# Kernel optimization log

Measured on AMD Instinct MI355X. Metric: run time of the kernel, lower is better.

The kernel has to match this reference:

```python
import jax, jax.numpy as jnp
import numpy as np

N, E, G = 40000, 640000, 64
IN, H, OUT = 128, 256, 128


def setup_inputs() -> dict:
    key = jax.random.key(0)
    ks = jax.random.split(key, 8)
    x = jax.random.normal(ks[0], (N, IN), dtype=jnp.float32)
    edge_index = jax.random.randint(ks[1], (2, E), 0, N, dtype=jnp.int64)
    batch = jnp.sort(jax.random.randint(ks[2], (N,), 0, G, dtype=jnp.int64))
    glorot = lambda k, sh: jax.random.normal(k, sh, jnp.float32) * (1.0 / np.sqrt(sh[0]))
    return {
        "x": x,
        "edge_index": edge_index,
        "batch": batch,
        "W_in": glorot(ks[3], (IN, H)), "b_in": jnp.zeros((H,), jnp.float32),
        "W_mid": glorot(ks[4], (H, H)), "b_mid": jnp.zeros((H,), jnp.float32),
        "W_out": glorot(ks[5], (H, OUT)), "b_out": jnp.zeros((OUT,), jnp.float32),
        "W_cls": glorot(ks[6], (OUT, 2)), "b_cls": jnp.zeros((2,), jnp.float32),
    }


def _gcn_conv(x, src, dst, deg_inv_sqrt, W, b):
    # PyG GCNConv: h = x @ W; propagate with symmetric norm (self-loops added); + bias
    h = x @ W
    norm = deg_inv_sqrt[src] * deg_inv_sqrt[dst]            # [E]
    agg = jax.ops.segment_sum(norm[:, None] * h[src], dst, num_segments=x.shape[0])
    agg = agg + (deg_inv_sqrt * deg_inv_sqrt)[:, None] * h  # self-loop contribution
    return agg + b


def reference(x, edge_index, batch, W_in, b_in, W_mid, b_mid, W_out, b_out, W_cls, b_cls):
    src, dst = edge_index[0], edge_index[1]
    n = x.shape[0]
    # degree with self-loops (in-degree on dst, matching PyG default flow)
    deg = jax.ops.segment_sum(jnp.ones((src.shape[0],), x.dtype), dst, num_segments=n) + 1.0
    dis = jax.lax.rsqrt(deg)

    h = jax.nn.relu(_gcn_conv(x, src, dst, dis, W_in, b_in))
    h = jax.nn.relu(_gcn_conv(h, src, dst, dis, W_mid, b_mid))   # num_layers - 2 = 1 middle layer
    node_embeddings = _gcn_conv(h, src, dst, dis, W_out, b_out)

    # global mean pool over graphs
    counts = jax.ops.segment_sum(jnp.ones((n,), x.dtype), batch, num_segments=G)
    graph_embedding = jax.ops.segment_sum(node_embeddings, batch, num_segments=G) / jnp.maximum(counts, 1.0)[:, None]

    logits = graph_embedding @ W_cls + b_cls
    return (node_embeddings, graph_embedding, logits)
```

## Files before the change

### kernel.cpp

```cpp
#include <hip/hip_runtime.h>
#include <hip/hip_bf16.h>

#define Nn   40000
#define Ee   640000
#define Gg   64
#define INF  128
#define Hh   256
#define OUTF 128

#define NBLK_N 157

typedef _Float16 half8 __attribute__((ext_vector_type(8)));
typedef float    f32x4 __attribute__((ext_vector_type(4)));

__global__ __launch_bounds__(256) void k_count(const int* __restrict__ dst, int* __restrict__ cnt) {
    int e = blockIdx.x * 256 + threadIdx.x;
    if (e < Ee) atomicAdd(&cnt[dst[e]], 1);
}

__global__ __launch_bounds__(256) void k_dis(const int* __restrict__ cnt, float* __restrict__ dis) {
    int i = blockIdx.x * 256 + threadIdx.x;
    if (i < Nn) dis[i] = rsqrtf((float)cnt[i] + 1.0f);
}

__global__ __launch_bounds__(256)
void k_scan1(const int* __restrict__ cnt, int* __restrict__ offs, int* __restrict__ partial) {
    __shared__ int sm[256];
    int i = blockIdx.x * 256 + threadIdx.x;
    int v = (i < Nn) ? cnt[i] : 0;
    sm[threadIdx.x] = v;
    __syncthreads();
#pragma unroll
    for (int d = 1; d < 256; d <<= 1) {
        int t = (threadIdx.x >= d) ? sm[threadIdx.x - d] : 0;
        __syncthreads();
        sm[threadIdx.x] += t;
        __syncthreads();
    }
    if (i < Nn) offs[i] = sm[threadIdx.x] - v;
    if (threadIdx.x == 255) partial[blockIdx.x] = sm[255];
}

__global__ __launch_bounds__(256)
void k_scan2(int* __restrict__ partial) {
    __shared__ int sm[256];
    int v = (threadIdx.x < NBLK_N) ? partial[threadIdx.x] : 0;
    sm[threadIdx.x] = v;
    __syncthreads();
#pragma unroll
    for (int d = 1; d < 256; d <<= 1) {
        int t = (threadIdx.x >= d) ? sm[threadIdx.x - d] : 0;
        __syncthreads();
        sm[threadIdx.x] += t;
        __syncthreads();
    }
    if (threadIdx.x < NBLK_N) partial[threadIdx.x] = sm[threadIdx.x] - v;
}

__global__ __launch_bounds__(256)
void k_scan3(int* __restrict__ offs, const int* __restrict__ partial) {
    int i = blockIdx.x * 256 + threadIdx.x;
    if (i < Nn) offs[i] += partial[blockIdx.x];
    if (i == 0) offs[Nn] = Ee;
}

__global__ __launch_bounds__(256)
void k_fill(const int* __restrict__ src, const int* __restrict__ dst,
            const int* __restrict__ offs, int* __restrict__ cursor,
            unsigned short* __restrict__ src_sorted) {
    int e = blockIdx.x * 256 + threadIdx.x;
    if (e >= Ee) return;
    int d = dst[e];
    int pos = offs[d] + atomicAdd(&cursor[d], 1);
    src_sorted[pos] = (unsigned short)src[e];
}

__global__ __launch_bounds__(256)
void k_cvt_x(const float* __restrict__ x, _Float16* __restrict__ xh) {
    int i = (blockIdx.x * 256 + threadIdx.x) * 4;
    if (i >= Nn * INF) return;
    float4 v = *(const float4*)&x[i];
    xh[i + 0] = (_Float16)v.x;
    xh[i + 1] = (_Float16)v.y;
    xh[i + 2] = (_Float16)v.z;
    xh[i + 3] = (_Float16)v.w;
}

__global__ __launch_bounds__(256)
void k_cvt_wt(const float* __restrict__ W, _Float16* __restrict__ Wt, int K, int N) {
    int idx = blockIdx.x * 256 + threadIdx.x;
    if (idx >= K * N) return;
    int n = idx / K;
    int k = idx - n * K;
    Wt[idx] = (_Float16)W[(size_t)k * N + n];
}

__global__ __launch_bounds__(256)
void k_gemm_mfma(const _Float16* __restrict__ A, const _Float16* __restrict__ Wt,
                 const float* __restrict__ dis, _Float16* __restrict__ C16,
                 int M, int N, int K) {
    __shared__ _Float16 Alds[128 * 40];
    __shared__ _Float16 Blds[128 * 40];
    const int tid = threadIdx.x;
    const int lane = tid & 63;
    const int waveId = tid >> 6;
    const int waveRow = waveId >> 1;
    const int waveCol = waveId & 1;
    const int quad = lane >> 4;
    const int m16 = lane & 15;
    const int rowBase = blockIdx.x * 128;
    const int colBase = blockIdx.y * 128;

    const int sRow  = tid >> 1;
    const int sKoff = (tid & 1) * 16;

    int gr = rowBase + sRow; if (gr >= M) gr = M - 1;
    const int gn = colBase + sRow;

    f32x4 acc[4][4];
#pragma unroll
    for (int i = 0; i < 4; ++i)
#pragma unroll
        for (int j = 0; j < 4; ++j)
            acc[i][j] = (f32x4){0.0f, 0.0f, 0.0f, 0.0f};

    for (int k0 = 0; k0 < K; k0 += 32) {
        const uint4* ap = (const uint4*)(A  + (size_t)gr * K + k0 + sKoff);
        const uint4* bp = (const uint4*)(Wt + (size_t)gn * K + k0 + sKoff);
        uint4 a0 = ap[0], a1 = ap[1];
        uint4 b0 = bp[0], b1 = bp[1];
        __syncthreads();
        *(uint4*)&Alds[sRow * 40 + sKoff]     = a0;
        *(uint4*)&Alds[sRow * 40 + sKoff + 8] = a1;
        *(uint4*)&Blds[sRow * 40 + sKoff]     = b0;
        *(uint4*)&Blds[sRow * 40 + sKoff + 8] = b1;
        __syncthreads();

        half8 a_frag[4], b_frag[4];
#pragma unroll
        for (int rt = 0; rt < 4; ++rt)
            a_frag[rt] = *(const half8*)&Alds[(waveRow * 64 + rt * 16 + m16) * 40 + quad * 8];
#pragma unroll
        for (int ct = 0; ct < 4; ++ct)
            b_frag[ct] = *(const half8*)&Blds[(waveCol * 64 + ct * 16 + m16) * 40 + quad * 8];
#pragma unroll
        for (int rt = 0; rt < 4; ++rt)
#pragma unroll
            for (int ct = 0; ct < 4; ++ct)
                acc[rt][ct] = __builtin_amdgcn_mfma_f32_16x16x32_f16(
                    a_frag[rt], b_frag[ct], acc[rt][ct], 0, 0, 0);
    }

#pragma unroll
    for (int rt = 0; rt < 4; ++rt) {
        const int rb = rowBase + waveRow * 64 + rt * 16 + quad * 4;
#pragma unroll
        for (int r = 0; r < 4; ++r) {
            const int row = rb + r;
            if (row < M) {
                const float s = dis[row];
#pragma unroll
                for (int ct = 0; ct < 4; ++ct) {
                    const int col = colBase + waveCol * 64 + ct * 16 + m16;
                    C16[(size_t)row * N + col] = (_Float16)(s * acc[rt][ct][r]);
                }
            }
        }
    }
}

template <int HH, bool RELU, bool H16OUT>
__global__ __launch_bounds__(256)
void k_gatherh(const int* __restrict__ offs, const unsigned short* __restrict__ srcs,
               const float* __restrict__ dis, const _Float16* __restrict__ hp,
               const float* __restrict__ bias, void* __restrict__ outv) {
    constexpr int V = HH / 64;
    typedef _Float16 halfv __attribute__((ext_vector_type(V)));
    int n = blockIdx.x * 4 + (threadIdx.x >> 6);
    if (n >= Nn) return;
    int lane = threadIdx.x & 63;
    int col = lane * V;
    int b = __builtin_amdgcn_readfirstlane(offs[n]);
    int e = __builtin_amdgcn_readfirstlane(offs[n + 1]);

    float acc[V];
    {
        halfv sv = *(const halfv*)(hp + (size_t)n * HH + col);
#pragma unroll
        for (int j = 0; j < V; ++j) acc[j] = (float)sv[j];
    }

    int i = b;
    for (; i + 4 <= e; i += 4) {
        int s0 = srcs[i], s1 = srcs[i + 1], s2 = srcs[i + 2], s3 = srcs[i + 3];
        halfv v0 = *(const halfv*)(hp + (size_t)s0 * HH + col);
        halfv v1 = *(const halfv*)(hp + (size_t)s1 * HH + col);
        halfv v2 = *(const halfv*)(hp + (size_t)s2 * HH + col);
        halfv v3 = *(const halfv*)(hp + (size_t)s3 * HH + col);
#pragma unroll
        for (int j = 0; j < V; ++j)
            acc[j] += (float)v0[j] + (float)v1[j] + (float)v2[j] + (float)v3[j];
    }
    for (; i < e; ++i) {
        int s0 = srcs[i];
        halfv v0 = *(const halfv*)(hp + (size_t)s0 * HH + col);
#pragma unroll
        for (int j = 0; j < V; ++j) acc[j] += (float)v0[j];
    }

    float dn = dis[n];
    float r[V];
#pragma unroll
    for (int j = 0; j < V; ++j) {
        r[j] = dn * acc[j] + bias[col + j];
        if (RELU) r[j] = fmaxf(r[j], 0.0f);
    }
    if constexpr (H16OUT) {
        halfv hv;
#pragma unroll
        for (int j = 0; j < V; ++j) hv[j] = (_Float16)r[j];
        *(halfv*)((_Float16*)outv + (size_t)n * HH + col) = hv;
    } else {
        if constexpr (V == 4) {
            *(float4*)((float*)outv + (size_t)n * HH + col) = make_float4(r[0], r[1], r[2], r[3]);
        } else {
            *(float2*)((float*)outv + (size_t)n * HH + col) = make_float2(r[0], r[1]);
        }
    }
}

__global__ __launch_bounds__(256)
void k_pool_accum(const float* __restrict__ emb, const int* __restrict__ batch,
                  float* __restrict__ ge_accum) {
    int n0 = blockIdx.x * 64;
    int nend = min(n0 + 64, Nn);
    int sub = threadIdx.x >> 6;
    int col = (threadIdx.x & 63) * 2;
    float ax = 0.0f, ay = 0.0f;
    int cur_g = -1;
    for (int n = n0 + sub; n < nend; n += 4) {
        int g = batch[n];
        if (g != cur_g) {
            if (cur_g >= 0) {
                unsafeAtomicAdd(&ge_accum[cur_g * OUTF + col], ax);
                unsafeAtomicAdd(&ge_accum[cur_g * OUTF + col + 1], ay);
            }
            cur_g = g; ax = 0.0f; ay = 0.0f;
        }
        float2 v = *(const float2*)&emb[(size_t)n * OUTF + col];
        ax += v.x; ay += v.y;
    }
    if (cur_g >= 0) {
        unsafeAtomicAdd(&ge_accum[cur_g * OUTF + col], ax);
        unsafeAtomicAdd(&ge_accum[cur_g * OUTF + col + 1], ay);
    }
}

__global__ __launch_bounds__(256)
void k_pool_div(const float* __restrict__ ge_accum, const int* __restrict__ batch,
                float* __restrict__ ge) {
    int idx = blockIdx.x * 256 + threadIdx.x;
    if (idx >= Gg * OUTF) return;
    int g = idx >> 7;
    int lo = 0, hi = Nn;
    while (lo < hi) { int mid = (lo + hi) >> 1; if (batch[mid] < g) lo = mid + 1; else hi = mid; }
    int start = lo;
    hi = Nn;
    while (lo < hi) { int mid = (lo + hi) >> 1; if (batch[mid] < g + 1) lo = mid + 1; else hi = mid; }
    float cnt = (float)(lo - start);
    ge[idx] = ge_accum[idx] / fmaxf(cnt, 1.0f);
}

__global__ __launch_bounds__(128)
void k_logits(const float* __restrict__ ge, const float* __restrict__ Wc,
              const float* __restrict__ bc, float* __restrict__ out) {
    int t = threadIdx.x;
    int g = t >> 1, c = t & 1;
    float s = bc[c];
    for (int k = 0; k < 128; ++k) s += ge[g * 128 + k] * Wc[k * 2 + c];
    out[t] = s;
}

extern "C" void kernel_launch(void* const* d_in, const int* in_sizes, int n_in,
                              void* d_out, int out_size, void* d_ws, size_t ws_size,
                              hipStream_t stream) {
    const float* x     = (const float*)d_in[0];
    const int*   ei    = (const int*)d_in[1];
    const int*   batch = (const int*)d_in[2];
    const float* W_in  = (const float*)d_in[3];
    const float* b_in  = (const float*)d_in[4];
    const float* W_mid = (const float*)d_in[5];
    const float* b_mid = (const float*)d_in[6];
    const float* W_out = (const float*)d_in[7];
    const float* b_out = (const float*)d_in[8];
    const float* W_cls = (const float*)d_in[9];
    const float* b_cls = (const float*)d_in[10];

    const int* src = ei;
    const int* dst = ei + Ee;

    float* ws = (float*)d_ws;
    float* dis      = ws;
    int*   cnt      = (int*)(ws + 40000);
    int*   offs     = (int*)(ws + 80000);
    int*   partial  = (int*)(ws + 120064);
    float* ge_accum = ws + 120256;
    unsigned short* src_sorted = (unsigned short*)(ws + 128448);
    _Float16* xh     = (_Float16*)(ws + 448448);
    _Float16* Wt_in  = (_Float16*)(ws + 3008448);
    _Float16* Wt_mid = (_Float16*)(ws + 3024832);
    _Float16* Wt_out = (_Float16*)(ws + 3057600);
    _Float16* hA     = (_Float16*)(ws + 3073984);
    _Float16* actA   = (_Float16*)(ws + 8193984);

    float* out    = (float*)d_out;
    float* ge_out = out + (size_t)Nn * OUTF;
    float* lg_out = ge_out + Gg * OUTF;

    const int nBlkE = (Ee + 255) / 256;
    const int gRows = (Nn + 127) / 128;
    const int nBlkG = (Nn + 3) / 4;

    hipMemsetAsync(cnt, 0, Nn * sizeof(int), stream);
    k_count<<<nBlkE, 256, 0, stream>>>(dst, cnt);
    k_dis<<<NBLK_N, 256, 0, stream>>>(cnt, dis);
    k_scan1<<<NBLK_N, 256, 0, stream>>>(cnt, offs, partial);
    k_scan2<<<1, 256, 0, stream>>>(partial);
    k_scan3<<<NBLK_N, 256, 0, stream>>>(offs, partial);
    hipMemsetAsync(cnt, 0, Nn * sizeof(int), stream);
    k_fill<<<nBlkE, 256, 0, stream>>>(src, dst, offs, cnt, src_sorted);

    k_cvt_x<<<(Nn * INF / 4 + 255) / 256, 256, 0, stream>>>(x, xh);
    k_cvt_wt<<<(INF * Hh + 255) / 256, 256, 0, stream>>>(W_in, Wt_in, INF, Hh);
    k_cvt_wt<<<(Hh * Hh + 255) / 256, 256, 0, stream>>>(W_mid, Wt_mid, Hh, Hh);
    k_cvt_wt<<<(Hh * OUTF + 255) / 256, 256, 0, stream>>>(W_out, Wt_out, Hh, OUTF);

    k_gemm_mfma<<<dim3(gRows, Hh / 128), 256, 0, stream>>>(xh, Wt_in, dis, hA, Nn, Hh, INF);
    k_gatherh<Hh, true, true><<<nBlkG, 256, 0, stream>>>(offs, src_sorted, dis, hA, b_in, actA);

    k_gemm_mfma<<<dim3(gRows, Hh / 128), 256, 0, stream>>>(actA, Wt_mid, dis, hA, Nn, Hh, Hh);
    k_gatherh<Hh, true, true><<<nBlkG, 256, 0, stream>>>(offs, src_sorted, dis, hA, b_mid, actA);

    k_gemm_mfma<<<dim3(gRows, OUTF / 128), 256, 0, stream>>>(actA, Wt_out, dis, hA, Nn, OUTF, Hh);
    k_gatherh<OUTF, false, false><<<nBlkG, 256, 0, stream>>>(offs, src_sorted, dis, hA, b_out, out);

    hipMemsetAsync(ge_accum, 0, Gg * OUTF * sizeof(float), stream);
    k_pool_accum<<<(Nn + 63) / 64, 256, 0, stream>>>(out, batch, ge_accum);
    k_pool_div<<<(Gg * OUTF + 255) / 256, 256, 0, stream>>>(ge_accum, batch, ge_out);
    k_logits<<<1, 128, 0, stream>>>(ge_out, W_cls, b_cls, lg_out);
}
```

Baseline: 361.8 us.

## Merge small setup and pooling kernels, drop memsets, use nontemporal gather loads

Folds the degree-inverse computation and the counter reset into the first scan kernel. It also merges the x and weight conversions plus the zeroing of the pool accumulator into one launch, and merges the pool division with the logits into a single-block kernel. This removes several kernel launches and two memsets. Separately, the neighbor gathers now use nontemporal loads, which risks losing cache reuse of the feature rows that are read repeatedly.

```diff
diff --git a/kernel.cpp b/kernel.cpp
--- a/kernel.cpp
+++ b/kernel.cpp
@@ -18,16 +18,17 @@
     if (e < Ee) atomicAdd(&cnt[dst[e]], 1);
 }
 
-__global__ __launch_bounds__(256) void k_dis(const int* __restrict__ cnt, float* __restrict__ dis) {
-    int i = blockIdx.x * 256 + threadIdx.x;
-    if (i < Nn) dis[i] = rsqrtf((float)cnt[i] + 1.0f);
-}
-
-__global__ __launch_bounds__(256)
-void k_scan1(const int* __restrict__ cnt, int* __restrict__ offs, int* __restrict__ partial) {
+__global__ __launch_bounds__(256)
+void k_scan1(int* __restrict__ cnt, int* __restrict__ offs, int* __restrict__ partial,
+             float* __restrict__ dis) {
     __shared__ int sm[256];
     int i = blockIdx.x * 256 + threadIdx.x;
-    int v = (i < Nn) ? cnt[i] : 0;
+    int v = 0;
+    if (i < Nn) {
+        v = cnt[i];
+        dis[i] = rsqrtf((float)v + 1.0f);
+        cnt[i] = 0;
+    }
     sm[threadIdx.x] = v;
     __syncthreads();
 #pragma unroll
@@ -76,23 +77,36 @@
 }
 
 __global__ __launch_bounds__(256)
-void k_cvt_x(const float* __restrict__ x, _Float16* __restrict__ xh) {
-    int i = (blockIdx.x * 256 + threadIdx.x) * 4;
-    if (i >= Nn * INF) return;
-    float4 v = *(const float4*)&x[i];
-    xh[i + 0] = (_Float16)v.x;
-    xh[i + 1] = (_Float16)v.y;
-    xh[i + 2] = (_Float16)v.z;
-    xh[i + 3] = (_Float16)v.w;
-}
-
-__global__ __launch_bounds__(256)
-void k_cvt_wt(const float* __restrict__ W, _Float16* __restrict__ Wt, int K, int N) {
-    int idx = blockIdx.x * 256 + threadIdx.x;
-    if (idx >= K * N) return;
-    int n = idx / K;
-    int k = idx - n * K;
-    Wt[idx] = (_Float16)W[(size_t)k * N + n];
+void k_cvt_all(const float* __restrict__ x, _Float16* __restrict__ xh,
+               const float* __restrict__ W_in,  _Float16* __restrict__ Wt_in,
+               const float* __restrict__ W_mid, _Float16* __restrict__ Wt_mid,
+               const float* __restrict__ W_out, _Float16* __restrict__ Wt_out,
+               float* __restrict__ ge_accum) {
+    int bid = blockIdx.x;
+    int tid = threadIdx.x;
+    if (bid < 5000) {
+        int i = (bid * 256 + tid) * 4;
+        float4 v = *(const float4*)&x[i];
+        xh[i + 0] = (_Float16)v.x;
+        xh[i + 1] = (_Float16)v.y;
+        xh[i + 2] = (_Float16)v.z;
+        xh[i + 3] = (_Float16)v.w;
+    } else if (bid < 5128) {
+        int idx = (bid - 5000) * 256 + tid;
+        int n = idx >> 7, k = idx & 127;
+        Wt_in[idx] = (_Float16)W_in[(size_t)k * Hh + n];
+    } else if (bid < 5384) {
+        int idx = (bid - 5128) * 256 + tid;
+        int n = idx >> 8, k = idx & 255;
+        Wt_mid[idx] = (_Float16)W_mid[(size_t)k * Hh + n];
+    } else if (bid < 5512) {
+        int idx = (bid - 5384) * 256 + tid;
+        int n = idx >> 8, k = idx & 255;
+        Wt_out[idx] = (_Float16)W_out[(size_t)k * OUTF + n];
+    } else {
+        int idx = (bid - 5512) * 256 + tid;
+        ge_accum[idx] = 0.0f;
+    }
 }
 
 __global__ __launch_bounds__(256)
@@ -183,6 +197,17 @@
     int b = __builtin_amdgcn_readfirstlane(offs[n]);
     int e = __builtin_amdgcn_readfirstlane(offs[n + 1]);
 
+    auto ldrow = [&](int s) -> halfv {
+        const _Float16* p = hp + (size_t)s * HH + col;
+        if constexpr (V == 4) {
+            unsigned long long u = __builtin_nontemporal_load((const unsigned long long*)p);
+            return __builtin_bit_cast(halfv, u);
+        } else {
+            unsigned int u = __builtin_nontemporal_load((const unsigned int*)p);
+            return __builtin_bit_cast(halfv, u);
+        }
+    };
+
     float acc[V];
     {
         halfv sv = *(const halfv*)(hp + (size_t)n * HH + col);
@@ -193,17 +218,16 @@
     int i = b;
     for (; i + 4 <= e; i += 4) {
         int s0 = srcs[i], s1 = srcs[i + 1], s2 = srcs[i + 2], s3 = srcs[i + 3];
-        halfv v0 = *(const halfv*)(hp + (size_t)s0 * HH + col);
-        halfv v1 = *(const halfv*)(hp + (size_t)s1 * HH + col);
-        halfv v2 = *(const halfv*)(hp + (size_t)s2 * HH + col);
-        halfv v3 = *(const halfv*)(hp + (size_t)s3 * HH + col);
+        halfv v0 = ldrow(s0);
+        halfv v1 = ldrow(s1);
+        halfv v2 = ldrow(s2);
+        halfv v3 = ldrow(s3);
 #pragma unroll
         for (int j = 0; j < V; ++j)
             acc[j] += (float)v0[j] + (float)v1[j] + (float)v2[j] + (float)v3[j];
     }
     for (; i < e; ++i) {
-        int s0 = srcs[i];
-        halfv v0 = *(const halfv*)(hp + (size_t)s0 * HH + col);
+        halfv v0 = ldrow(srcs[i]);
 #pragma unroll
         for (int j = 0; j < V; ++j) acc[j] += (float)v0[j];
     }
@@ -257,28 +281,32 @@
 }
 
 __global__ __launch_bounds__(256)
-void k_pool_div(const float* __restrict__ ge_accum, const int* __restrict__ batch,
-                float* __restrict__ ge) {
-    int idx = blockIdx.x * 256 + threadIdx.x;
-    if (idx >= Gg * OUTF) return;
-    int g = idx >> 7;
-    int lo = 0, hi = Nn;
-    while (lo < hi) { int mid = (lo + hi) >> 1; if (batch[mid] < g) lo = mid + 1; else hi = mid; }
-    int start = lo;
-    hi = Nn;
-    while (lo < hi) { int mid = (lo + hi) >> 1; if (batch[mid] < g + 1) lo = mid + 1; else hi = mid; }
-    float cnt = (float)(lo - start);
-    ge[idx] = ge_accum[idx] / fmaxf(cnt, 1.0f);
-}
-
-__global__ __launch_bounds__(128)
-void k_logits(const float* __restrict__ ge, const float* __restrict__ Wc,
-              const float* __restrict__ bc, float* __restrict__ out) {
+void k_pool_fin(const float* __restrict__ ge_accum, const int* __restrict__ batch,
+                const float* __restrict__ Wc, const float* __restrict__ bc,
+                float* __restrict__ ge_out, float* __restrict__ lg_out) {
+    __shared__ float ge_s[Gg * OUTF];
+    __shared__ int seg[Gg + 1];
     int t = threadIdx.x;
-    int g = t >> 1, c = t & 1;
-    float s = bc[c];
-    for (int k = 0; k < 128; ++k) s += ge[g * 128 + k] * Wc[k * 2 + c];
-    out[t] = s;
+    if (t <= Gg) {
+        int lo = 0, hi = Nn;
+        while (lo < hi) { int mid = (lo + hi) >> 1; if (batch[mid] < t) lo = mid + 1; else hi = mid; }
+        seg[t] = lo;
+    }
+    __syncthreads();
+    for (int idx = t; idx < Gg * OUTF; idx += 256) {
+        int g = idx >> 7;
+        float cnt = (float)(seg[g + 1] - seg[g]);
+        float v = ge_accum[idx] / fmaxf(cnt, 1.0f);
+        ge_s[idx] = v;
+        ge_out[idx] = v;
+    }
+    __syncthreads();
+    if (t < 128) {
+        int g = t >> 1, c = t & 1;
+        float s = bc[c];
+        for (int k = 0; k < 128; ++k) s += ge_s[g * 128 + k] * Wc[k * 2 + c];
+        lg_out[t] = s;
+    }
 }
 
 extern "C" void kernel_launch(void* const* d_in, const int* in_sizes, int n_in,
@@ -321,19 +349,14 @@
     const int gRows = (Nn + 127) / 128;
     const int nBlkG = (Nn + 3) / 4;
 
-    hipMemsetAsync(cnt, 0, Nn * sizeof(int), stream);
+    (void)hipMemsetAsync(cnt, 0, Nn * sizeof(int), stream);
     k_count<<<nBlkE, 256, 0, stream>>>(dst, cnt);
-    k_dis<<<NBLK_N, 256, 0, stream>>>(cnt, dis);
-    k_scan1<<<NBLK_N, 256, 0, stream>>>(cnt, offs, partial);
+    k_scan1<<<NBLK_N, 256, 0, stream>>>(cnt, offs, partial, dis);
     k_scan2<<<1, 256, 0, stream>>>(partial);
     k_scan3<<<NBLK_N, 256, 0, stream>>>(offs, partial);
-    hipMemsetAsync(cnt, 0, Nn * sizeof(int), stream);
     k_fill<<<nBlkE, 256, 0, stream>>>(src, dst, offs, cnt, src_sorted);
 
-    k_cvt_x<<<(Nn * INF / 4 + 255) / 256, 256, 0, stream>>>(x, xh);
-    k_cvt_wt<<<(INF * Hh + 255) / 256, 256, 0, stream>>>(W_in, Wt_in, INF, Hh);
-    k_cvt_wt<<<(Hh * Hh + 255) / 256, 256, 0, stream>>>(W_mid, Wt_mid, Hh, Hh);
-    k_cvt_wt<<<(Hh * OUTF + 255) / 256, 256, 0, stream>>>(W_out, Wt_out, Hh, OUTF);
+    k_cvt_all<<<5544, 256, 0, stream>>>(x, xh, W_in, Wt_in, W_mid, Wt_mid, W_out, Wt_out, ge_accum);
 
     k_gemm_mfma<<<dim3(gRows, Hh / 128), 256, 0, stream>>>(xh, Wt_in, dis, hA, Nn, Hh, INF);
     k_gatherh<Hh, true, true><<<nBlkG, 256, 0, stream>>>(offs, src_sorted, dis, hA, b_in, actA);
@@ -344,8 +367,6 @@
     k_gemm_mfma<<<dim3(gRows, OUTF / 128), 256, 0, stream>>>(actA, Wt_out, dis, hA, Nn, OUTF, Hh);
     k_gatherh<OUTF, false, false><<<nBlkG, 256, 0, stream>>>(offs, src_sorted, dis, hA, b_out, out);
 
-    hipMemsetAsync(ge_accum, 0, Gg * OUTF * sizeof(float), stream);
     k_pool_accum<<<(Nn + 63) / 64, 256, 0, stream>>>(out, batch, ge_accum);
-    k_pool_div<<<(Gg * OUTF + 255) / 256, 256, 0, stream>>>(ge_accum, batch, ge_out);
-    k_logits<<<1, 128, 0, stream>>>(ge_out, W_cls, b_cls, lg_out);
-}
+    k_pool_fin<<<1, 256, 0, stream>>>(ge_accum, batch, W_cls, b_cls, ge_out, lg_out);
+}
```

New measurement: 406.5 us. +12.3%, slower.
